# Performance work log

Measured on AMD Instinct MI355X. Metric: run time of the kernel, lower is better.

## Reference

```python
import jax, jax.numpy as jnp
import numpy as np

EPS = 1e-12
SIMILARITY = 'dot'  # non-tensor forward arg, closed over


def setup_inputs() -> dict:
    key = jax.random.key(0)
    k1, k2, k3, k4 = jax.random.split(key, 4)
    N, M, D = 4096, 8192, 512
    x = jax.random.normal(k1, (N, D), dtype=jnp.float32)
    x_n = jax.random.normal(k2, (M, D), dtype=jnp.float32)
    # Linear(D, 3) params
    W = jax.random.normal(k3, (3, D), dtype=jnp.float32) * (1.0 / np.sqrt(D))
    bias = jax.random.normal(k4, (3,), dtype=jnp.float32) * 0.01
    return {"x": x, "x_n": x_n, "W": W, "bias": bias}


def _sim_matrix(x, x_n, similarity):
    if similarity == 'l2':
        d2 = (jnp.sum(x * x, 1)[:, None] - 2.0 * (x @ x_n.T)
              + jnp.sum(x_n * x_n, 1)[None, :])
        return -jnp.sqrt(jnp.maximum(d2, 0.0))
    elif similarity == 'l1':
        return -jnp.sum(jnp.abs(x[:, None, :] - x_n[None, :, :]), axis=-1)
    elif similarity == 'dot':
        return (x @ x_n.T) / x.shape[1]
    elif similarity == 'cos':
        xn = x / jnp.linalg.norm(x, axis=1, keepdims=True)
        yn = x_n / jnp.linalg.norm(x_n, axis=1, keepdims=True)
        return xn @ yn.T


def reference(x, x_n, W, bias):
    # pointwise params from a Linear(D,3)+Sigmoid head, clamped to (eps, 1-eps)
    p = jnp.clip(jax.nn.sigmoid(x @ W.T + bias), EPS, 1.0 - EPS)  # [N,3]
    a = p[:, 0:1]
    b = p[:, 1:2]
    s = p[:, 2:3]
    b = a + b * (1.0 - a)

    sim = _sim_matrix(x, x_n, SIMILARITY)                # [N,M]
    smin = jnp.min(sim, axis=1, keepdims=True)
    smax = jnp.max(sim, axis=1, keepdims=True)
    sim_norm = (sim - smin) / (smax - smin)

    # x != x_n -> plain row max (torch.equal branch is False)
    top_sims = jnp.max(sim_norm, axis=1, keepdims=True)  # [N,1]
    a = jnp.minimum(a, top_sims) - EPS

    num = jnp.maximum(jnp.abs(sim_norm - a) ** (1.0 / s), EPS)
    denom = num + jnp.maximum(jnp.abs(b - sim_norm) ** (1.0 / s), EPS)
    soft_mask = num / denom

    lo = sim_norm < a
    hi = sim_norm > b
    soft_mask = jnp.where(lo, 0.0, jnp.where(hi, 1.0, soft_mask))
    # safe log: masked-to-0 entries give -inf forward, zero grad (matches torch)
    safe = jnp.where(lo, 1.0, soft_mask)
    log_mask = jnp.where(lo, -jnp.inf, jnp.log(safe))
    return sim + log_mask
```

## Files before the change

kernel.cpp:

```cpp
#include <hip/hip_runtime.h>
#include <hip/hip_fp16.h>
#include <math.h>

#define EPSF 1e-12f
#define NEG_HUGE (-1e30f)

typedef _Float16 half8_t __attribute__((ext_vector_type(8)));
typedef _Float16 half4_t __attribute__((ext_vector_type(4)));
typedef float floatx4 __attribute__((ext_vector_type(4)));

__device__ __forceinline__ float sigmoid_stable(float v) {
    if (v >= 0.0f) {
        return 1.0f / (1.0f + expf(-v));
    } else {
        float e = expf(v);
        return e / (1.0f + e);
    }
}

__global__ __launch_bounds__(64) void row_params_kernel(
    const float* __restrict__ x, const float* __restrict__ W,
    const float* __restrict__ bias,
    float* __restrict__ aeff, float* __restrict__ bnew, float* __restrict__ tinv)
{
    const int r = blockIdx.x;
    const int l = threadIdx.x;
    const float* xr = x + (size_t)r * 512;
    float s0 = 0.0f, s1 = 0.0f, s2 = 0.0f;
#pragma unroll
    for (int i = 0; i < 8; ++i) {
        int e = l * 8 + i;
        float xv = xr[e];
        s0 = fmaf(xv, W[e], s0);
        s1 = fmaf(xv, W[512 + e], s1);
        s2 = fmaf(xv, W[1024 + e], s2);
    }
#pragma unroll
    for (int off = 32; off > 0; off >>= 1) {
        s0 += __shfl_xor(s0, off);
        s1 += __shfl_xor(s1, off);
        s2 += __shfl_xor(s2, off);
    }
    if (l == 0) {
        float p0 = fminf(fmaxf(sigmoid_stable(s0 + bias[0]), EPSF), 1.0f);
        float p1 = fminf(fmaxf(sigmoid_stable(s1 + bias[1]), EPSF), 1.0f);
        float p2 = fminf(fmaxf(sigmoid_stable(s2 + bias[2]), EPSF), 1.0f);
        float b = p0 + p1 * (1.0f - p0);
        float ae = fminf(p0, 1.0f) - EPSF;
        aeff[r] = ae;
        bnew[r] = b;
        tinv[r] = 1.0f / p2;
    }
}

__global__ __launch_bounds__(256) void split_both_kernel(
    const float* __restrict__ x, const float* __restrict__ xn,
    _Float16* __restrict__ A2, _Float16* __restrict__ B2)
{
    int idx = blockIdx.x * 256 + threadIdx.x;
    int row = idx >> 7;
    int c = (idx & 127) << 2;
    const float* src;
    _Float16* dst;
    bool isB;
    if (row < 4096) {
        src = x + (size_t)row * 512 + c;
        dst = A2 + (size_t)row * 1536 + c;
        isB = false;
    } else {
        int r = row - 4096;
        src = xn + (size_t)r * 512 + c;
        dst = B2 + (size_t)r * 1536 + c;
        isB = true;
    }
    float4 v = *(const float4*)src;
    _Float16 h0 = (_Float16)v.x, h1 = (_Float16)v.y,
             h2 = (_Float16)v.z, h3 = (_Float16)v.w;
    half4_t hv = {h0, h1, h2, h3};
    half4_t lv = {(_Float16)(v.x - (float)h0), (_Float16)(v.y - (float)h1),
                  (_Float16)(v.z - (float)h2), (_Float16)(v.w - (float)h3)};
    *(half4_t*)(dst) = hv;
    *(half4_t*)(dst + 512)  = isB ? lv : hv;
    *(half4_t*)(dst + 1024) = isB ? hv : lv;
}

__device__ __forceinline__ void load_tile_row16(
    const _Float16* gbase, _Float16* lds_base, int lane)
{
    const _Float16* g = gbase + (size_t)(lane >> 2) * 1536 + (size_t)(lane & 3) * 8;
    __builtin_amdgcn_global_load_lds(
        (const __attribute__((address_space(1))) unsigned int*)g,
        (__attribute__((address_space(3))) unsigned int*)lds_base,
        16, 0, 0);
}

__global__ __launch_bounds__(256) void mfma_gemm_kernel(
    const _Float16* __restrict__ A, const _Float16* __restrict__ B,
    float* __restrict__ C,
    float* __restrict__ pmin, float* __restrict__ pmax)
{
    constexpr int Kp = 1536;
    constexpr int N = 8192;
    __shared__ __align__(16) _Float16 As[128 * 32];
    __shared__ __align__(16) _Float16 Bs[128 * 32];

    const int t = threadIdx.x;
    const int wave = t >> 6;
    const int lane = t & 63;
    const int bx = blockIdx.x;
    const int by = blockIdx.y;

    const _Float16* Abase = A + (size_t)(by * 128 + wave * 16) * Kp;
    const _Float16* Bbase = B + (size_t)(bx * 128 + wave * 16) * Kp;
    _Float16* AsW0 = &As[(wave * 16) * 32];
    _Float16* AsW1 = &As[(64 + wave * 16) * 32];
    _Float16* BsW0 = &Bs[(wave * 16) * 32];
    _Float16* BsW1 = &Bs[(64 + wave * 16) * 32];
    const size_t rs64 = (size_t)64 * Kp;

    const int wm = (wave >> 1) * 64;
    const int wn = (wave & 1) * 64;
    const _Float16* aptr = &As[(wm + (lane & 15)) * 32 + (lane >> 4) * 8];
    const _Float16* bptr = &Bs[(wn + (lane & 15)) * 32 + (lane >> 4) * 8];

    floatx4 acc[4][4] = {};

    for (int kt = 0; kt < Kp / 32; ++kt) {
        const _Float16* Ak = Abase + kt * 32;
        const _Float16* Bk = Bbase + kt * 32;
        load_tile_row16(Ak, AsW0, lane);
        load_tile_row16(Ak + rs64, AsW1, lane);
        load_tile_row16(Bk, BsW0, lane);
        load_tile_row16(Bk + rs64, BsW1, lane);
        __syncthreads();

        half8_t af[4], bf[4];
#pragma unroll
        for (int i = 0; i < 4; ++i) af[i] = *(const half8_t*)(aptr + i * 16 * 32);
#pragma unroll
        for (int j = 0; j < 4; ++j) bf[j] = *(const half8_t*)(bptr + j * 16 * 32);
#pragma unroll
        for (int i = 0; i < 4; ++i)
#pragma unroll
            for (int j = 0; j < 4; ++j)
                acc[i][j] = __builtin_amdgcn_mfma_f32_16x16x32_f16(
                    af[i], bf[j], acc[i][j], 0, 0, 0);
        __syncthreads();
    }

    const float sc = 1.0f / 512.0f;
    const int row0 = by * 128 + wm + (lane >> 4) * 4;
    const int col0 = bx * 128 + wn + (lane & 15);
#pragma unroll
    for (int i = 0; i < 4; ++i) {
#pragma unroll
        for (int r = 0; r < 4; ++r) {
            float* cp = C + (size_t)(row0 + i * 16 + r) * N + col0;
#pragma unroll
            for (int j = 0; j < 4; ++j)
                cp[j * 16] = acc[i][j][r] * sc;
        }
    }

    float mnv[4][4], mxv[4][4];
#pragma unroll
    for (int i = 0; i < 4; ++i)
#pragma unroll
        for (int r = 0; r < 4; ++r) {
            float lo = fminf(fminf(acc[i][0][r], acc[i][1][r]),
                             fminf(acc[i][2][r], acc[i][3][r]));
            float hi = fmaxf(fmaxf(acc[i][0][r], acc[i][1][r]),
                             fmaxf(acc[i][2][r], acc[i][3][r]));
            mnv[i][r] = lo * sc;
            mxv[i][r] = hi * sc;
        }
#pragma unroll
    for (int off = 1; off < 16; off <<= 1)
#pragma unroll
        for (int i = 0; i < 4; ++i)
#pragma unroll
            for (int r = 0; r < 4; ++r) {
                mnv[i][r] = fminf(mnv[i][r], __shfl_xor(mnv[i][r], off));
                mxv[i][r] = fmaxf(mxv[i][r], __shfl_xor(mxv[i][r], off));
            }
    if ((lane & 15) == 0) {
        const int pb = bx * 2 + (wave & 1);
#pragma unroll
        for (int i = 0; i < 4; ++i)
#pragma unroll
            for (int r = 0; r < 4; ++r) {
                size_t row = (size_t)(row0 + i * 16 + r);
                pmin[(row << 7) + pb] = mnv[i][r];
                pmax[(row << 7) + pb] = mxv[i][r];
            }
    }
}

__global__ __launch_bounds__(64) void minmax_reduce_kernel(
    const float* __restrict__ pmin, const float* __restrict__ pmax,
    float* __restrict__ smin, float* __restrict__ smax)
{
    const int r = blockIdx.x;
    const int l = threadIdx.x;
    const float* bmin = pmin + ((size_t)r << 7);
    const float* bmax = pmax + ((size_t)r << 7);
    float mn = fminf(bmin[l], bmin[l + 64]);
    float mx = fmaxf(bmax[l], bmax[l + 64]);
#pragma unroll
    for (int off = 32; off > 0; off >>= 1) {
        mn = fminf(mn, __shfl_xor(mn, off));
        mx = fmaxf(mx, __shfl_xor(mx, off));
    }
    if (l == 0) {
        smin[r] = mn;
        smax[r] = mx;
    }
}

#define BM 128
#define BN 128
#define BK 16
__global__ __launch_bounds__(256) void sgemm_nt_kernel(
    const float* __restrict__ A, const float* __restrict__ B,
    float* __restrict__ C)
{
    const int K = 512;
    const int N = 8192;
    __shared__ float As[BK][BM];
    __shared__ float Bs[BK][BN];
    const int t = threadIdx.x;
    const int bx = blockIdx.x, by = blockIdx.y;
    const int m0 = t >> 2;
    const int kq = (t & 3) << 2;
    const float* Ap = A + ((size_t)(by * BM + m0) * K + kq);
    const float* Bp = B + ((size_t)(bx * BN + m0) * K + kq);
    const int tx = t & 15, ty = t >> 4;
    float acc[8][8] = {};
    float4 a0 = *(const float4*)(Ap), a1 = *(const float4*)(Ap + (size_t)64 * K);
    float4 b0 = *(const float4*)(Bp), b1 = *(const float4*)(Bp + (size_t)64 * K);
    for (int kt = 0; kt < K / BK; ++kt) {
        As[kq + 0][m0] = a0.x; As[kq + 1][m0] = a0.y; As[kq + 2][m0] = a0.z; As[kq + 3][m0] = a0.w;
        As[kq + 0][m0 + 64] = a1.x; As[kq + 1][m0 + 64] = a1.y; As[kq + 2][m0 + 64] = a1.z; As[kq + 3][m0 + 64] = a1.w;
        Bs[kq + 0][m0] = b0.x; Bs[kq + 1][m0] = b0.y; Bs[kq + 2][m0] = b0.z; Bs[kq + 3][m0] = b0.w;
        Bs[kq + 0][m0 + 64] = b1.x; Bs[kq + 1][m0 + 64] = b1.y; Bs[kq + 2][m0 + 64] = b1.z; Bs[kq + 3][m0 + 64] = b1.w;
        __syncthreads();
        if (kt + 1 < K / BK) {
            const float* Ap2 = Ap + (size_t)(kt + 1) * BK;
            const float* Bp2 = Bp + (size_t)(kt + 1) * BK;
            a0 = *(const float4*)(Ap2); a1 = *(const float4*)(Ap2 + (size_t)64 * K);
            b0 = *(const float4*)(Bp2); b1 = *(const float4*)(Bp2 + (size_t)64 * K);
        }
#pragma unroll
        for (int k = 0; k < BK; ++k) {
            float4 xa0 = *(const float4*)(&As[k][ty * 8]);
            float4 xa1 = *(const float4*)(&As[k][ty * 8 + 4]);
            float4 yb0 = *(const float4*)(&Bs[k][tx * 8]);
            float4 yb1 = *(const float4*)(&Bs[k][tx * 8 + 4]);
            float av[8] = {xa0.x, xa0.y, xa0.z, xa0.w, xa1.x, xa1.y, xa1.z, xa1.w};
            float bv[8] = {yb0.x, yb0.y, yb0.z, yb0.w, yb1.x, yb1.y, yb1.z, yb1.w};
#pragma unroll
            for (int i = 0; i < 8; ++i)
#pragma unroll
                for (int j = 0; j < 8; ++j)
                    acc[i][j] = fmaf(av[i], bv[j], acc[i][j]);
        }
        __syncthreads();
    }
    const float sc = 1.0f / 512.0f;
    const int gm = by * BM + ty * 8, gn = bx * BN + tx * 8;
#pragma unroll
    for (int i = 0; i < 8; ++i) {
        float4 o0 = make_float4(acc[i][0] * sc, acc[i][1] * sc, acc[i][2] * sc, acc[i][3] * sc);
        float4 o1 = make_float4(acc[i][4] * sc, acc[i][5] * sc, acc[i][6] * sc, acc[i][7] * sc);
        float* cp = C + (size_t)(gm + i) * N + gn;
        *(float4*)(cp) = o0;
        *(float4*)(cp + 4) = o1;
    }
}

__global__ __launch_bounds__(256) void row_minmax_kernel(
    const float* __restrict__ C, float* __restrict__ smin, float* __restrict__ smax)
{
    const int r = blockIdx.x;
    const float4* row = (const float4*)(C + (size_t)r * 8192);
    float mn = INFINITY, mx = -INFINITY;
#pragma unroll
    for (int i = 0; i < 8; ++i) {
        float4 v = row[threadIdx.x + i * 256];
        mn = fminf(mn, fminf(fminf(v.x, v.y), fminf(v.z, v.w)));
        mx = fmaxf(mx, fmaxf(fmaxf(v.x, v.y), fmaxf(v.z, v.w)));
    }
#pragma unroll
    for (int off = 32; off > 0; off >>= 1) {
        mn = fminf(mn, __shfl_xor(mn, off));
        mx = fmaxf(mx, __shfl_xor(mx, off));
    }
    __shared__ float smn[4], smx[4];
    if ((threadIdx.x & 63) == 0) {
        smn[threadIdx.x >> 6] = mn;
        smx[threadIdx.x >> 6] = mx;
    }
    __syncthreads();
    if (threadIdx.x == 0) {
        mn = fminf(fminf(smn[0], smn[1]), fminf(smn[2], smn[3]));
        mx = fmaxf(fmaxf(smx[0], smx[1]), fmaxf(smx[2], smx[3]));
        smin[r] = mn;
        smax[r] = mx;
    }
}

__device__ __forceinline__ float fast_pow(float x, float t) {
    return __expf(t * __logf(x));
}

__global__ __launch_bounds__(256) void epilogue_kernel(
    float* __restrict__ C,
    const float* __restrict__ aeff, const float* __restrict__ bnew,
    const float* __restrict__ tinv,
    const float* __restrict__ smin, const float* __restrict__ smax)
{
    const int r = blockIdx.y;
    const int c4 = blockIdx.x * 256 + threadIdx.x;
    const float a = aeff[r];
    const float b = bnew[r];
    const float t = tinv[r];
    const float mn = smin[r];
    const float range = smax[r] - mn;
    const float inv_range = (range > 0.0f) ? (1.0f / range) : 0.0f;

    floatx4* p = (floatx4*)(C + (size_t)r * 8192) + c4;
    floatx4 v = __builtin_nontemporal_load(p);
    floatx4 out;
#pragma unroll
    for (int i = 0; i < 4; ++i) {
        float sim = v[i];
        float sn = (sim - mn) * inv_range;
        float lm;
        if (sn < a) {
            lm = NEG_HUGE;
        } else if (sn > b) {
            lm = 0.0f;
        } else {
            float num = fmaxf(fast_pow(fabsf(sn - a), t), EPSF);
            float den = num + fmaxf(fast_pow(fabsf(b - sn), t), EPSF);
            lm = __logf(num / den);
        }
        out[i] = sim + lm;
    }
    __builtin_nontemporal_store(out, p);
}

extern "C" void kernel_launch(void* const* d_in, const int* in_sizes, int n_in,
                              void* d_out, int out_size, void* d_ws, size_t ws_size,
                              hipStream_t stream)
{
    const float* x    = (const float*)d_in[0];
    const float* x_n  = (const float*)d_in[1];
    const float* W    = (const float*)d_in[2];
    const float* bias = (const float*)d_in[3];
    float* C = (float*)d_out;
    float* ws = (float*)d_ws;

    float* aeff = ws;
    float* bnew = ws + 4096;
    float* tinv = ws + 8192;
    float* smin = ws + 12288;
    float* smax = ws + 16384;

    const size_t pmin_off = 128 * 1024;
    const size_t pbytes = (size_t)4096 * 128 * 4;
    const size_t a2_off = pmin_off + 2 * pbytes;
    const size_t a2_bytes = (size_t)4096 * 1536 * 2;
    const size_t b2_off = a2_off + a2_bytes;
    const size_t need = b2_off + (size_t)8192 * 1536 * 2;

    row_params_kernel<<<4096, 64, 0, stream>>>(x, W, bias, aeff, bnew, tinv);

    if (ws_size >= need) {
        float* pmin = (float*)((char*)d_ws + pmin_off);
        float* pmax = (float*)((char*)d_ws + pmin_off + pbytes);
        _Float16* A2 = (_Float16*)((char*)d_ws + a2_off);
        _Float16* B2 = (_Float16*)((char*)d_ws + b2_off);
        split_both_kernel<<<6144, 256, 0, stream>>>(x, x_n, A2, B2);
        mfma_gemm_kernel<<<dim3(64, 32), 256, 0, stream>>>(A2, B2, C, pmin, pmax);
        minmax_reduce_kernel<<<4096, 64, 0, stream>>>(pmin, pmax, smin, smax);
    } else {
        sgemm_nt_kernel<<<dim3(8192 / BN, 4096 / BM), 256, 0, stream>>>(x, x_n, C);
        row_minmax_kernel<<<4096, 256, 0, stream>>>(C, smin, smax);
    }

    epilogue_kernel<<<dim3(8, 4096), 256, 0, stream>>>(C, aeff, bnew, tinv,
                                                       smin, smax);
}
```

Baseline: 326.5 us.

## Fuse row-params into split kernel, shrink split buffers, reduce min/max in-block

The fp16 hi/lo split now writes each row once as [hi|lo] with stride 1024 instead of three 512-wide segments with stride 1536. The GEMM walks three passes over it (hi*hi, hi*lo, lo*hi) with offset pointers, so the same K work reads less workspace and the split kernel writes a third fewer bytes. The row-parameter head is folded into the split kernel as extra blocks, which removes one launch. The GEMM also combines its two wave partials per row through LDS before storing a column-major partial array, so the final min/max reduction kernel runs with coalesced reads and far fewer blocks.

```diff
diff --git a/kernel.cpp b/kernel.cpp
--- a/kernel.cpp
+++ b/kernel.cpp
@@ -18,76 +18,72 @@
     }
 }
 
-__global__ __launch_bounds__(64) void row_params_kernel(
-    const float* __restrict__ x, const float* __restrict__ W,
-    const float* __restrict__ bias,
+__global__ __launch_bounds__(256) void split_params_kernel(
+    const float* __restrict__ x, const float* __restrict__ xn,
+    const float* __restrict__ W, const float* __restrict__ bias,
+    _Float16* __restrict__ A2, _Float16* __restrict__ B2,
     float* __restrict__ aeff, float* __restrict__ bnew, float* __restrict__ tinv)
 {
-    const int r = blockIdx.x;
-    const int l = threadIdx.x;
-    const float* xr = x + (size_t)r * 512;
-    float s0 = 0.0f, s1 = 0.0f, s2 = 0.0f;
-#pragma unroll
-    for (int i = 0; i < 8; ++i) {
-        int e = l * 8 + i;
-        float xv = xr[e];
-        s0 = fmaf(xv, W[e], s0);
-        s1 = fmaf(xv, W[512 + e], s1);
-        s2 = fmaf(xv, W[1024 + e], s2);
-    }
-#pragma unroll
-    for (int off = 32; off > 0; off >>= 1) {
-        s0 += __shfl_xor(s0, off);
-        s1 += __shfl_xor(s1, off);
-        s2 += __shfl_xor(s2, off);
-    }
-    if (l == 0) {
-        float p0 = fminf(fmaxf(sigmoid_stable(s0 + bias[0]), EPSF), 1.0f);
-        float p1 = fminf(fmaxf(sigmoid_stable(s1 + bias[1]), EPSF), 1.0f);
-        float p2 = fminf(fmaxf(sigmoid_stable(s2 + bias[2]), EPSF), 1.0f);
-        float b = p0 + p1 * (1.0f - p0);
-        float ae = fminf(p0, 1.0f) - EPSF;
-        aeff[r] = ae;
-        bnew[r] = b;
-        tinv[r] = 1.0f / p2;
-    }
-}
-
-__global__ __launch_bounds__(256) void split_both_kernel(
-    const float* __restrict__ x, const float* __restrict__ xn,
-    _Float16* __restrict__ A2, _Float16* __restrict__ B2)
-{
-    int idx = blockIdx.x * 256 + threadIdx.x;
-    int row = idx >> 7;
-    int c = (idx & 127) << 2;
-    const float* src;
-    _Float16* dst;
-    bool isB;
-    if (row < 4096) {
-        src = x + (size_t)row * 512 + c;
-        dst = A2 + (size_t)row * 1536 + c;
-        isB = false;
+    const int blk = blockIdx.x;
+    const int t = threadIdx.x;
+    if (blk < 6144) {
+        int idx = blk * 256 + t;
+        int row = idx >> 7;
+        int c = (idx & 127) << 2;
+        const float* src;
+        _Float16* dst;
+        if (row < 4096) {
+            src = x + (size_t)row * 512 + c;
+            dst = A2 + (size_t)row * 1024 + c;
+        } else {
+            int r = row - 4096;
+            src = xn + (size_t)r * 512 + c;
+            dst = B2 + (size_t)r * 1024 + c;
+        }
+        float4 v = *(const float4*)src;
+        _Float16 h0 = (_Float16)v.x, h1 = (_Float16)v.y,
+                 h2 = (_Float16)v.z, h3 = (_Float16)v.w;
+        half4_t hv = {h0, h1, h2, h3};
+        half4_t lv = {(_Float16)(v.x - (float)h0), (_Float16)(v.y - (float)h1),
+                      (_Float16)(v.z - (float)h2), (_Float16)(v.w - (float)h3)};
+        *(half4_t*)(dst) = hv;
+        *(half4_t*)(dst + 512) = lv;
     } else {
-        int r = row - 4096;
-        src = xn + (size_t)r * 512 + c;
-        dst = B2 + (size_t)r * 1536 + c;
-        isB = true;
-    }
-    float4 v = *(const float4*)src;
-    _Float16 h0 = (_Float16)v.x, h1 = (_Float16)v.y,
-             h2 = (_Float16)v.z, h3 = (_Float16)v.w;
-    half4_t hv = {h0, h1, h2, h3};
-    half4_t lv = {(_Float16)(v.x - (float)h0), (_Float16)(v.y - (float)h1),
-                  (_Float16)(v.z - (float)h2), (_Float16)(v.w - (float)h3)};
-    *(half4_t*)(dst) = hv;
-    *(half4_t*)(dst + 512)  = isB ? lv : hv;
-    *(half4_t*)(dst + 1024) = isB ? hv : lv;
+        const int r = (blk - 6144) * 4 + (t >> 6);
+        const int l = t & 63;
+        const float* xr = x + (size_t)r * 512;
+        float s0 = 0.0f, s1 = 0.0f, s2 = 0.0f;
+#pragma unroll
+        for (int i = 0; i < 8; ++i) {
+            int e = l * 8 + i;
+            float xv = xr[e];
+            s0 = fmaf(xv, W[e], s0);
+            s1 = fmaf(xv, W[512 + e], s1);
+            s2 = fmaf(xv, W[1024 + e], s2);
+        }
+#pragma unroll
+        for (int off = 32; off > 0; off >>= 1) {
+            s0 += __shfl_xor(s0, off);
+            s1 += __shfl_xor(s1, off);
+            s2 += __shfl_xor(s2, off);
+        }
+        if (l == 0) {
+            float p0 = fminf(fmaxf(sigmoid_stable(s0 + bias[0]), EPSF), 1.0f);
+            float p1 = fminf(fmaxf(sigmoid_stable(s1 + bias[1]), EPSF), 1.0f);
+            float p2 = fminf(fmaxf(sigmoid_stable(s2 + bias[2]), EPSF), 1.0f);
+            float b = p0 + p1 * (1.0f - p0);
+            float ae = fminf(p0, 1.0f) - EPSF;
+            aeff[r] = ae;
+            bnew[r] = b;
+            tinv[r] = 1.0f / p2;
+        }
+    }
 }
 
 __device__ __forceinline__ void load_tile_row16(
     const _Float16* gbase, _Float16* lds_base, int lane)
 {
-    const _Float16* g = gbase + (size_t)(lane >> 2) * 1536 + (size_t)(lane & 3) * 8;
+    const _Float16* g = gbase + (size_t)(lane >> 2) * 1024 + (size_t)(lane & 3) * 8;
     __builtin_amdgcn_global_load_lds(
         (const __attribute__((address_space(1))) unsigned int*)g,
         (__attribute__((address_space(3))) unsigned int*)lds_base,
@@ -99,7 +95,7 @@
     float* __restrict__ C,
     float* __restrict__ pmin, float* __restrict__ pmax)
 {
-    constexpr int Kp = 1536;
+    constexpr int Kp = 1024;
     constexpr int N = 8192;
     __shared__ __align__(16) _Float16 As[128 * 32];
     __shared__ __align__(16) _Float16 Bs[128 * 32];
@@ -125,31 +121,36 @@
 
     floatx4 acc[4][4] = {};
 
-    for (int kt = 0; kt < Kp / 32; ++kt) {
-        const _Float16* Ak = Abase + kt * 32;
-        const _Float16* Bk = Bbase + kt * 32;
-        load_tile_row16(Ak, AsW0, lane);
-        load_tile_row16(Ak + rs64, AsW1, lane);
-        load_tile_row16(Bk, BsW0, lane);
-        load_tile_row16(Bk + rs64, BsW1, lane);
-        __syncthreads();
-
-        half8_t af[4], bf[4];
-#pragma unroll
-        for (int i = 0; i < 4; ++i) af[i] = *(const half8_t*)(aptr + i * 16 * 32);
-#pragma unroll
-        for (int j = 0; j < 4; ++j) bf[j] = *(const half8_t*)(bptr + j * 16 * 32);
-#pragma unroll
-        for (int i = 0; i < 4; ++i)
-#pragma unroll
-            for (int j = 0; j < 4; ++j)
-                acc[i][j] = __builtin_amdgcn_mfma_f32_16x16x32_f16(
-                    af[i], bf[j], acc[i][j], 0, 0, 0);
-        __syncthreads();
+    for (int p = 0; p < 3; ++p) {
+        const _Float16* Ap = Abase + ((p == 2) ? 512 : 0);
+        const _Float16* Bp = Bbase + ((p == 1) ? 512 : 0);
+        for (int k2 = 0; k2 < 16; ++k2) {
+            const _Float16* Ak = Ap + k2 * 32;
+            const _Float16* Bk = Bp + k2 * 32;
+            load_tile_row16(Ak, AsW0, lane);
+            load_tile_row16(Ak + rs64, AsW1, lane);
+            load_tile_row16(Bk, BsW0, lane);
+            load_tile_row16(Bk + rs64, BsW1, lane);
+            __syncthreads();
+
+            half8_t af[4], bf[4];
+#pragma unroll
+            for (int i = 0; i < 4; ++i) af[i] = *(const half8_t*)(aptr + i * 16 * 32);
+#pragma unroll
+            for (int j = 0; j < 4; ++j) bf[j] = *(const half8_t*)(bptr + j * 16 * 32);
+#pragma unroll
+            for (int i = 0; i < 4; ++i)
+#pragma unroll
+                for (int j = 0; j < 4; ++j)
+                    acc[i][j] = __builtin_amdgcn_mfma_f32_16x16x32_f16(
+                        af[i], bf[j], acc[i][j], 0, 0, 0);
+            __syncthreads();
+        }
     }
 
     const float sc = 1.0f / 512.0f;
-    const int row0 = by * 128 + wm + (lane >> 4) * 4;
+    const int lrow0 = wm + (lane >> 4) * 4;
+    const int row0 = by * 128 + lrow0;
     const int col0 = bx * 128 + wn + (lane & 15);
 #pragma unroll
     for (int i = 0; i < 4; ++i) {
@@ -183,35 +184,48 @@
                 mnv[i][r] = fminf(mnv[i][r], __shfl_xor(mnv[i][r], off));
                 mxv[i][r] = fmaxf(mxv[i][r], __shfl_xor(mxv[i][r], off));
             }
+    float* lmin = (float*)As;
+    float* lmax = lmin + 256;
     if ((lane & 15) == 0) {
-        const int pb = bx * 2 + (wave & 1);
 #pragma unroll
         for (int i = 0; i < 4; ++i)
 #pragma unroll
             for (int r = 0; r < 4; ++r) {
-                size_t row = (size_t)(row0 + i * 16 + r);
-                pmin[(row << 7) + pb] = mnv[i][r];
-                pmax[(row << 7) + pb] = mxv[i][r];
+                int row = lrow0 + i * 16 + r;
+                lmin[row * 2 + (wave & 1)] = mnv[i][r];
+                lmax[row * 2 + (wave & 1)] = mxv[i][r];
             }
     }
-}
-
-__global__ __launch_bounds__(64) void minmax_reduce_kernel(
+    __syncthreads();
+    if (t < 128) {
+        float mn = fminf(lmin[t * 2], lmin[t * 2 + 1]);
+        float mx = fmaxf(lmax[t * 2], lmax[t * 2 + 1]);
+        pmin[(size_t)bx * 4096 + by * 128 + t] = mn;
+        pmax[(size_t)bx * 4096 + by * 128 + t] = mx;
+    }
+}
+
+__global__ __launch_bounds__(256) void minmax_reduce_kernel(
     const float* __restrict__ pmin, const float* __restrict__ pmax,
     float* __restrict__ smin, float* __restrict__ smax)
 {
-    const int r = blockIdx.x;
-    const int l = threadIdx.x;
-    const float* bmin = pmin + ((size_t)r << 7);
-    const float* bmax = pmax + ((size_t)r << 7);
-    float mn = fminf(bmin[l], bmin[l + 64]);
-    float mx = fmaxf(bmax[l], bmax[l + 64]);
-#pragma unroll
-    for (int off = 32; off > 0; off >>= 1) {
-        mn = fminf(mn, __shfl_xor(mn, off));
-        mx = fmaxf(mx, __shfl_xor(mx, off));
-    }
-    if (l == 0) {
+    const int t = threadIdx.x;
+    const int r = blockIdx.x * 64 + (t & 63);
+    const int g = t >> 6;
+    float mn = INFINITY, mx = -INFINITY;
+#pragma unroll
+    for (int i = 0; i < 16; ++i) {
+        int bx = g * 16 + i;
+        mn = fminf(mn, pmin[(size_t)bx * 4096 + r]);
+        mx = fmaxf(mx, pmax[(size_t)bx * 4096 + r]);
+    }
+    __shared__ float sm[4][64], sx[4][64];
+    sm[g][t & 63] = mn;
+    sx[g][t & 63] = mx;
+    __syncthreads();
+    if (t < 64) {
+        mn = fminf(fminf(sm[0][t], sm[1][t]), fminf(sm[2][t], sm[3][t]));
+        mx = fmaxf(fmaxf(sx[0][t], sx[1][t]), fmaxf(sx[2][t], sx[3][t]));
         smin[r] = mn;
         smax[r] = mx;
     }
@@ -309,6 +323,41 @@
     }
 }
 
+__global__ __launch_bounds__(64) void row_params_kernel(
+    const float* __restrict__ x, const float* __restrict__ W,
+    const float* __restrict__ bias,
+    float* __restrict__ aeff, float* __restrict__ bnew, float* __restrict__ tinv)
+{
+    const int r = blockIdx.x;
+    const int l = threadIdx.x;
+    const float* xr = x + (size_t)r * 512;
+    float s0 = 0.0f, s1 = 0.0f, s2 = 0.0f;
+#pragma unroll
+    for (int i = 0; i < 8; ++i) {
+        int e = l * 8 + i;
+        float xv = xr[e];
+        s0 = fmaf(xv, W[e], s0);
+        s1 = fmaf(xv, W[512 + e], s1);
+        s2 = fmaf(xv, W[1024 + e], s2);
+    }
+#pragma unroll
+    for (int off = 32; off > 0; off >>= 1) {
+        s0 += __shfl_xor(s0, off);
+        s1 += __shfl_xor(s1, off);
+        s2 += __shfl_xor(s2, off);
+    }
+    if (l == 0) {
+        float p0 = fminf(fmaxf(sigmoid_stable(s0 + bias[0]), EPSF), 1.0f);
+        float p1 = fminf(fmaxf(sigmoid_stable(s1 + bias[1]), EPSF), 1.0f);
+        float p2 = fminf(fmaxf(sigmoid_stable(s2 + bias[2]), EPSF), 1.0f);
+        float b = p0 + p1 * (1.0f - p0);
+        float ae = fminf(p0, 1.0f) - EPSF;
+        aeff[r] = ae;
+        bnew[r] = b;
+        tinv[r] = 1.0f / p2;
+    }
+}
+
 __device__ __forceinline__ float fast_pow(float x, float t) {
     return __expf(t * __logf(x));
 }
@@ -368,23 +417,23 @@
     float* smax = ws + 16384;
 
     const size_t pmin_off = 128 * 1024;
-    const size_t pbytes = (size_t)4096 * 128 * 4;
+    const size_t pbytes = (size_t)64 * 4096 * 4;
     const size_t a2_off = pmin_off + 2 * pbytes;
-    const size_t a2_bytes = (size_t)4096 * 1536 * 2;
+    const size_t a2_bytes = (size_t)4096 * 1024 * 2;
     const size_t b2_off = a2_off + a2_bytes;
-    const size_t need = b2_off + (size_t)8192 * 1536 * 2;
-
-    row_params_kernel<<<4096, 64, 0, stream>>>(x, W, bias, aeff, bnew, tinv);
+    const size_t need = b2_off + (size_t)8192 * 1024 * 2;
 
     if (ws_size >= need) {
         float* pmin = (float*)((char*)d_ws + pmin_off);
         float* pmax = (float*)((char*)d_ws + pmin_off + pbytes);
         _Float16* A2 = (_Float16*)((char*)d_ws + a2_off);
         _Float16* B2 = (_Float16*)((char*)d_ws + b2_off);
-        split_both_kernel<<<6144, 256, 0, stream>>>(x, x_n, A2, B2);
+        split_params_kernel<<<7168, 256, 0, stream>>>(x, x_n, W, bias, A2, B2,
+                                                      aeff, bnew, tinv);
         mfma_gemm_kernel<<<dim3(64, 32), 256, 0, stream>>>(A2, B2, C, pmin, pmax);
-        minmax_reduce_kernel<<<4096, 64, 0, stream>>>(pmin, pmax, smin, smax);
+        minmax_reduce_kernel<<<64, 256, 0, stream>>>(pmin, pmax, smin, smax);
     } else {
+        row_params_kernel<<<4096, 64, 0, stream>>>(x, W, bias, aeff, bnew, tinv);
         sgemm_nt_kernel<<<dim3(8192 / BN, 4096 / BM), 256, 0, stream>>>(x, x_n, C);
         row_minmax_kernel<<<4096, 256, 0, stream>>>(C, smin, smax);
     }
```

Result: slower. 333.1 us (+2.0%).
